# Optimization experiments

Measured on AMD Instinct MI355X. Metric: run time of the kernel, lower is better.

## Reference

```python
import jax, jax.numpy as jnp
import numpy as np

H, DK, DV = 4, 64, 64        # heads, key/value head dims (hidden=256)
M, TOPK = 4, 2               # num memories, router top-k
GN, EPS, COND_SCALE = 16.0, 1e-5, 1.0


def setup_inputs() -> dict:
    key = jax.random.key(0)
    ks = jax.random.split(key, 12)
    B, Q, K, D = 8, 64, 256, 256
    w = lambda k, shape, fan: jax.random.normal(k, shape, jnp.float32) / np.sqrt(fan).astype(np.float32)
    return {
        "query": jax.random.normal(ks[0], (B, Q, D), jnp.float32),
        "keyval": jax.random.normal(ks[1], (B, K, D), jnp.float32),
        "attention_mask_kv": jnp.ones((B, K), jnp.int32),
        "W_cond": w(ks[2], (D, D), D),
        "W_q": w(ks[3], (D, H * DK), D),
        "W_k": w(ks[4], (D, H * DK), D),
        "W_v": w(ks[5], (D, H * DV), D),
        "W_gk1": w(ks[6], (D, 16), D),
        "W_gk2": w(ks[7], (16, H * DK), 16),
        "b_gk2": jnp.zeros((H * DK,), jnp.float32),
        "W_router": w(ks[8], (D, M), D),
        "norm_w": jnp.ones((DV,), jnp.float32),
        "W_o": w(ks[9], (H * DV, D), H * DV),
    }


def _mem_last(q_last, k, v, gk, sel, wgt):
    """Last-token output of one gated linear-attention memory.
    S_t = diag(exp(gk_t)) S_{t-1} + k_t v_t^T ; o_T = q_T S_T.
    q_last: (N,H,DK); k,gk: (N,K,H,DK); v: (N,K,H,DV); sel,wgt: (N,K)."""
    k_e = k * sel[:, :, None, None]
    v_e = v * wgt[:, :, None, None]
    gk_e = gk * sel[:, :, None, None]          # unselected tokens: no decay, no update
    G = jnp.cumsum(gk_e, axis=1)               # (N,K,H,DK), log decays
    decay = jnp.exp(G[:, -1:, :, :] - G)       # remaining decay to last step, <= 1
    s = jnp.einsum('nhd,nthd->nth', q_last, k_e * decay)
    return jnp.einsum('nth,nthv->nhv', s, v_e)


def reference(query, keyval, attention_mask_kv, W_cond, W_q, W_k, W_v,
              W_gk1, W_gk2, b_gk2, W_router, norm_w, W_o):
    B, Q, D = query.shape
    K = keyval.shape[1]
    N = B * Q
    # broadcast KV expansion + cond injection
    cond = (query @ W_cond) * COND_SCALE                         # (B,Q,D)
    x = (keyval[:, None, :, :] + cond[:, :, None, :]).reshape(N, K, D)
    m = jnp.broadcast_to(attention_mask_kv[:, None, :].astype(x.dtype), (B, Q, K)).reshape(N, K)
    # projections
    q = (x @ W_q).reshape(N, K, H, DK)
    k = (x @ W_k).reshape(N, K, H, DK) * m[:, :, None, None]
    v = (x @ W_v).reshape(N, K, H, DV) * m[:, :, None, None]
    gk = (jax.nn.log_sigmoid(x @ W_gk1 @ W_gk2 + b_gk2) / GN).reshape(N, K, H, DK)
    gk = gk * m[:, :, None, None]
    # router: softmax -> top-k -> renormalize
    router_logits = (x @ W_router).reshape(N * K, M)
    probs = jax.nn.softmax(router_logits, axis=-1)
    topv, topi = jax.lax.top_k(probs, TOPK)
    topv = topv / jnp.sum(topv, axis=-1, keepdims=True)
    w_mem = jnp.sum(jax.nn.one_hot(topi, M, dtype=x.dtype) * topv[..., None], axis=-2)
    w_mem = w_mem.reshape(N, K, M)
    # shared memory (always on) + routed memories
    q_last = q[:, -1]
    ones = jnp.ones((N, K), x.dtype)
    o = _mem_last(q_last, k, v, gk, ones, ones)
    for e in range(M):
        we = w_mem[:, :, e]
        o = o + _mem_last(q_last, k, v, gk, (we > 0).astype(x.dtype), we)
    # per-head RMSNorm + output projection
    o = o * jax.lax.rsqrt(jnp.mean(o * o, axis=-1, keepdims=True) + EPS) * norm_w
    out = (o.reshape(N, H * DV) @ W_o).reshape(B, Q, D)
    return out, router_logits
```

## Files before the change

kernel.cpp:

```cpp
#include <hip/hip_runtime.h>
#include <math.h>

#define Hh   4
#define Bb   8
#define Qq   64
#define Kk   256
#define Dd   256
#define Nn   (Bb * Qq)
#define GNf  16.0f
#define EPSf 1e-5f

#define SKV  832
#define SCB  1088

__device__ __forceinline__ float wred(float x) {
#pragma unroll
    for (int off = 32; off > 0; off >>= 1)
        x += __shfl_xor(x, off, 64);
    return x;
}

__global__ __launch_bounds__(256) void prep(
    const float* __restrict__ Wg1, const float* __restrict__ Wg2,
    float* __restrict__ Wg)
{
    const int e = blockIdx.x * 256 + threadIdx.x;
    const int k = e >> 8, c = e & 255;
    float s = 0.f;
#pragma unroll
    for (int i = 0; i < 16; ++i)
        s = fmaf(Wg1[k * 16 + i], Wg2[i * 256 + c], s);
    Wg[e] = s;
}

__device__ __forceinline__ void gemm_tile(
    const float* __restrict__ A, int lda, int Mv,
    const float* __restrict__ B, int ldb, int bn,
    float* __restrict__ C, int ldc)
{
    __shared__ float As[16][68];
    __shared__ float Ws[16][136];
    const int tid = threadIdx.x;
    const int ty = tid >> 4, tx = tid & 15;
    const int am = tid >> 2, ak = (tid & 3) << 2;
    const int wk = tid >> 4, wc = (tid & 15) << 3;
    const int ams = (am < Mv) ? am : (Mv - 1);

    float acc[4][8] = {};

    const float* aptr = A + (size_t)ams * lda + ak;
    const float* bptr = B + (size_t)wk * ldb + bn + wc;
    float4 av  = *(const float4*)(aptr);
    float4 bv0 = *(const float4*)(bptr);
    float4 bv1 = *(const float4*)(bptr + 4);

    for (int k0 = 0; k0 < 256; k0 += 16) {
        __syncthreads();
        As[ak + 0][am] = av.x;
        As[ak + 1][am] = av.y;
        As[ak + 2][am] = av.z;
        As[ak + 3][am] = av.w;
        *(float4*)&Ws[wk][wc]     = bv0;
        *(float4*)&Ws[wk][wc + 4] = bv1;
        __syncthreads();
        if (k0 + 16 < 256) {
            av  = *(const float4*)(aptr + k0 + 16);
            bv0 = *(const float4*)(bptr + (size_t)(k0 + 16) * ldb);
            bv1 = *(const float4*)(bptr + (size_t)(k0 + 16) * ldb + 4);
        }
#pragma unroll
        for (int kk = 0; kk < 16; ++kk) {
            const float4 a4 = *(const float4*)&As[kk][ty << 2];
            const float4 w0 = *(const float4*)&Ws[kk][tx << 2];
            const float4 w1 = *(const float4*)&Ws[kk][64 + (tx << 2)];
            const float a_[4] = {a4.x, a4.y, a4.z, a4.w};
            const float w_[8] = {w0.x, w0.y, w0.z, w0.w, w1.x, w1.y, w1.z, w1.w};
#pragma unroll
            for (int i = 0; i < 4; ++i)
#pragma unroll
                for (int jj = 0; jj < 8; ++jj)
                    acc[i][jj] = fmaf(a_[i], w_[jj], acc[i][jj]);
        }
    }

#pragma unroll
    for (int i = 0; i < 4; ++i) {
        const int rr = (ty << 2) + i;
        if (rr < Mv) {
            *(float4*)(C + (size_t)rr * ldc + (tx << 2)) =
                make_float4(acc[i][0], acc[i][1], acc[i][2], acc[i][3]);
            *(float4*)(C + (size_t)rr * ldc + 64 + (tx << 2)) =
                make_float4(acc[i][4], acc[i][5], acc[i][6], acc[i][7]);
        }
    }
}

__device__ __forceinline__ void router_region(
    const float* __restrict__ A, const float* __restrict__ Wr,
    float* __restrict__ C, int ldc, int row0)
{
    __shared__ float WrT[4][260];
    const int tid = threadIdx.x;
    for (int idx = tid; idx < 1024; idx += 256) {
        const int k = idx >> 2, c = idx & 3;
        WrT[c][k] = Wr[idx];
    }
    __syncthreads();
    const int row = row0 + (tid >> 2), c = tid & 3;
    const float* a = A + (size_t)row * 256;
    float acc = 0.f;
#pragma unroll 8
    for (int k4 = 0; k4 < 64; ++k4) {
        const float4 avv = *(const float4*)(a + (k4 << 2));
        const float4 wvv = *(const float4*)&WrT[c][k4 << 2];
        acc = fmaf(avv.x, wvv.x, acc);
        acc = fmaf(avv.y, wvv.y, acc);
        acc = fmaf(avv.z, wvv.z, acc);
        acc = fmaf(avv.w, wvv.w, acc);
    }
    C[(size_t)row * ldc + c] = acc;
}

__global__ __launch_bounds__(256) void gemm_main(
    const float* __restrict__ keyval, const float* __restrict__ query,
    const float* __restrict__ W_k, const float* __restrict__ W_v,
    const float* __restrict__ Wg, const float* __restrict__ W_cond,
    const float* __restrict__ W_q, const float* __restrict__ W_router,
    float* __restrict__ KVb, float* __restrict__ cond,
    float* __restrict__ qlast)
{
    const int id = blockIdx.x;
    if (id < 242 - 32) {
        const float* A; int lda, Mv; const float* Bm; int bn; float* C; int ldc;
        if (id < 192) {
            const int rt = id / 6, ct = id % 6;
            const float* Bsel; int cbase;
            if (ct < 2)      { Bsel = W_k; cbase = 0; }
            else if (ct < 4) { Bsel = W_v; cbase = 256; }
            else             { Bsel = Wg;  cbase = 512; }
            A = keyval + (size_t)rt * 64 * 256; lda = 256; Mv = 64;
            Bm = Bsel; bn = (ct & 1) * 128;
            C = KVb + (size_t)rt * 64 * SKV + cbase + bn; ldc = SKV;
        } else if (id < 208) {
            const int t = id - 192, rt = t >> 1, ct = t & 1;
            A = query + (size_t)rt * 64 * 256; lda = 256; Mv = 64;
            Bm = W_cond; bn = ct * 128;
            C = cond + (size_t)rt * 64 * 256 + ct * 128; ldc = 256;
        } else {
            const int ct = id - 208;
            A = keyval + 255 * 256; lda = Kk * Dd; Mv = 8;
            Bm = W_q; bn = ct * 128;
            C = qlast + ct * 128; ldc = 256;
        }
        gemm_tile(A, lda, Mv, Bm, 256, bn, C, ldc);
    } else {
        router_region(keyval, W_router, KVb + 768, SKV, (id - 210) * 64);
    }
}

__global__ __launch_bounds__(256) void gemm_cb(
    const float* __restrict__ cond,
    const float* __restrict__ W_q, const float* __restrict__ W_k,
    const float* __restrict__ W_v, const float* __restrict__ Wg,
    const float* __restrict__ W_router, float* __restrict__ Cb)
{
    const int id = blockIdx.x;
    if (id < 64) {
        const int rg = id >> 4, t = id & 15, rt = t >> 1, ct = t & 1;
        const float* Bsel = (rg == 0) ? W_q : (rg == 1) ? W_k : (rg == 2) ? W_v : Wg;
        gemm_tile(cond + (size_t)rt * 64 * 256, 256, 64,
                  Bsel, 256, ct * 128,
                  Cb + (size_t)rt * 64 * SCB + rg * 256 + ct * 128, SCB);
    } else {
        router_region(cond, W_router, Cb + 1024, SCB, (id - 64) * 64);
    }
}

__global__ __launch_bounds__(256) void mom_fused(
    const float* __restrict__ KVb, const float* __restrict__ Cb,
    const float* __restrict__ qlast, const float* __restrict__ b_gk2,
    const int* __restrict__ mask, const float* __restrict__ W_o,
    const float* __restrict__ norm_w, float* __restrict__ out,
    float* __restrict__ logits)
{
    __shared__ float4 wm[Kk];
    __shared__ float4 sw[Kk];
    __shared__ float  smf[Kk];
    __shared__ float  Ptile[4][16][68];
    __shared__ float  sbuf[4][16];
    __shared__ float  onorm[Dd];

    const int bid = blockIdx.x;
    const int n = ((bid & 7) << 6) | (bid >> 3);
    const int b = n >> 6;
    const int j = threadIdx.x;
    const int lane = j & 63;
    const int wv = j >> 6;

    const float qc = Cb[(size_t)n * SCB + j];
    const float kc = Cb[(size_t)n * SCB + 256 + j];
    const float vc = Cb[(size_t)n * SCB + 512 + j];
    const float pc = Cb[(size_t)n * SCB + 768 + j] + b_gk2[j];
    const float4 rc = *(const float4*)(Cb + (size_t)n * SCB + 1024);

    const int* pm = mask + b * Kk;

    {
        const float4 kvr = *(const float4*)(KVb + (size_t)(b * Kk + j) * SKV + 768);
        float l[4] = {kvr.x + rc.x, kvr.y + rc.y, kvr.z + rc.z, kvr.w + rc.w};
        *(float4*)(logits + ((size_t)n * Kk + j) * 4) = make_float4(l[0], l[1], l[2], l[3]);

        int i1 = 0;
#pragma unroll
        for (int q = 1; q < 4; ++q) if (l[q] > l[i1]) i1 = q;
        int i2 = -1;
#pragma unroll
        for (int q = 0; q < 4; ++q) {
            if (q == i1) continue;
            if (i2 < 0 || l[q] > l[i2]) i2 = q;
        }
        const float mx = fmaxf(l[i1], l[i2]);
        const float e1 = __expf(l[i1] - mx);
        const float e2 = __expf(l[i2] - mx);
        const float inv = 1.f / (e1 + e2);
        float w[4] = {0.f, 0.f, 0.f, 0.f};
        w[i1] = e1 * inv;
        w[i2] = e2 * inv;
        wm[j] = make_float4(w[0], w[1], w[2], w[3]);
        const float mfj = (float)pm[j];
        smf[j] = mfj;
        sw[j] = make_float4(w[0] > 0.f ? mfj : 0.f, w[1] > 0.f ? mfj : 0.f,
                            w[2] > 0.f ? mfj : 0.f, w[3] > 0.f ? mfj : 0.f);
    }
    __syncthreads();

    const float ql  = qlast[b * Dd + j] + qc;
    const float qkc = ql * kc;
    const float* pkv = KVb + (size_t)b * Kk * SKV + j;

    float E0 = 1.f, E1 = 1.f, E2 = 1.f, E3 = 1.f, E4 = 1.f;
    float o = 0.f;
    const int tl = lane & 15, qq = lane >> 4;

    for (int t0 = Kk - 16; t0 >= 0; t0 -= 16) {
        float vreg[16];
#pragma unroll
        for (int i = 0; i < 16; ++i) {
            const int t = t0 + 15 - i;
            const float* r = pkv + (size_t)t * SKV;
            const float kraw = r[0];
            const float vraw = r[256];
            const float praw = r[512];
            const float pre = praw + pc;
            const float ee = __expf(-pre);
            const float dg = __expf(-0.0625f * __logf(1.0f + ee));
            const float4 w  = wm[t];
            const float4 s4 = sw[t];
            const float mf  = smf[t];
            const float zf = E0 + w.x * E1 + w.y * E2 + w.z * E3 + w.w * E4;
            const float qlk = fmaf(ql, kraw, qkc);
            Ptile[wv][i][lane] = qlk * zf * mf;
            vreg[i] = vraw + vc;
            const float d1 = dg - 1.0f;
            E0 *= fmaf(mf,   d1, 1.0f);
            E1 *= fmaf(s4.x, d1, 1.0f);
            E2 *= fmaf(s4.y, d1, 1.0f);
            E3 *= fmaf(s4.z, d1, 1.0f);
            E4 *= fmaf(s4.w, d1, 1.0f);
        }
        __builtin_amdgcn_wave_barrier();

        float s = 0.f;
#pragma unroll
        for (int rr = 0; rr < 4; ++rr) {
            const float4 p4 = *(const float4*)&Ptile[wv][tl][qq * 16 + rr * 4];
            s += (p4.x + p4.y) + (p4.z + p4.w);
        }
        s += __shfl_xor(s, 16, 64);
        s += __shfl_xor(s, 32, 64);
        sbuf[wv][tl] = s;
        __builtin_amdgcn_wave_barrier();
#pragma unroll
        for (int rr = 0; rr < 4; ++rr) {
            const float4 sv = *(const float4*)&sbuf[wv][rr * 4];
            o = fmaf(sv.x, vreg[rr * 4 + 0], o);
            o = fmaf(sv.y, vreg[rr * 4 + 1], o);
            o = fmaf(sv.z, vreg[rr * 4 + 2], o);
            o = fmaf(sv.w, vreg[rr * 4 + 3], o);
        }
    }

    const float ms = wred(o * o) * (1.0f / 64.0f);
    onorm[j] = o * rsqrtf(ms + EPSf) * norm_w[lane];
    __syncthreads();

    float acc = 0.f;
#pragma unroll 8
    for (int k = 0; k < Dd; ++k)
        acc = fmaf(onorm[k], W_o[(size_t)k * Dd + j], acc);
    out[(size_t)n * Dd + j] = acc;
}

extern "C" void kernel_launch(void* const* d_in, const int* in_sizes, int n_in,
                              void* d_out, int out_size, void* d_ws, size_t ws_size,
                              hipStream_t stream)
{
    const float* query    = (const float*)d_in[0];
    const float* keyval   = (const float*)d_in[1];
    const int*   mask     = (const int*)  d_in[2];
    const float* W_cond   = (const float*)d_in[3];
    const float* W_q      = (const float*)d_in[4];
    const float* W_k      = (const float*)d_in[5];
    const float* W_v      = (const float*)d_in[6];
    const float* W_gk1    = (const float*)d_in[7];
    const float* W_gk2    = (const float*)d_in[8];
    const float* b_gk2    = (const float*)d_in[9];
    const float* W_router = (const float*)d_in[10];
    const float* norm_w   = (const float*)d_in[11];
    const float* W_o      = (const float*)d_in[12];

    float* out    = (float*)d_out;
    float* logits = out + Nn * Dd;

    float* p = (float*)d_ws;
    float* Wg    = p; p += 256 * 256;
    float* KVb   = p; p += 2048 * SKV;
    float* cond  = p; p += Nn * 256;
    float* qlast = p; p += 8 * 256;
    float* Cb    = p; p += Nn * SCB;

    prep<<<256, dim3(256), 0, stream>>>(W_gk1, W_gk2, Wg);

    gemm_main<<<242, dim3(256), 0, stream>>>(
        keyval, query, W_k, W_v, Wg, W_cond, W_q, W_router, KVb, cond, qlast);

    gemm_cb<<<72, dim3(256), 0, stream>>>(cond, W_q, W_k, W_v, Wg, W_router, Cb);

    mom_fused<<<Nn, dim3(256), 0, stream>>>(
        KVb, Cb, qlast, b_gk2, mask, W_o, norm_w, out, logits);
}
```

Measured before the change: 206.0 us.

## Fuse all stages into one persistent kernel with software grid barriers

Merges the weight-prep, the keyval/cond projection GEMMs and the memory recurrence into a single 512-block kernel. Stages are separated by atomic-counter grid barriers, and shared memory is shared through a union. The projection GEMMs move to 128x128 tiles, and the gating selection masks are now computed inline instead of staged through shared arrays. This removes three launch boundaries and the tail gaps between them. In exchange it relies on all 512 blocks being co-resident (launch_bounds 256,2) to avoid deadlock, and leaves many blocks idle during the early phases.

```diff
diff --git a/kernel.cpp b/kernel.cpp
--- a/kernel.cpp
+++ b/kernel.cpp
@@ -10,8 +10,19 @@
 #define GNf  16.0f
 #define EPSf 1e-5f
 
-#define SKV  832
-#define SCB  1088
+#define SKV  776
+#define SCB  1032
+#define GRID 512
+
+struct MomS {
+    float4 wm[Kk];
+    float  Pt[4][16][68];
+    float  sbuf[4][16];
+    float  onorm[Dd];
+};
+struct GemmS { float As[16][136]; float Ws[16][136]; };
+struct RtrS  { float WrT[4][260]; };
+union  AllS  { MomS m; GemmS g; RtrS r; };
 
 __device__ __forceinline__ float wred(float x) {
 #pragma unroll
@@ -20,26 +31,24 @@
     return x;
 }
 
-__global__ __launch_bounds__(256) void prep(
-    const float* __restrict__ Wg1, const float* __restrict__ Wg2,
-    float* __restrict__ Wg)
-{
-    const int e = blockIdx.x * 256 + threadIdx.x;
-    const int k = e >> 8, c = e & 255;
-    float s = 0.f;
-#pragma unroll
-    for (int i = 0; i < 16; ++i)
-        s = fmaf(Wg1[k * 16 + i], Wg2[i * 256 + c], s);
-    Wg[e] = s;
-}
-
-__device__ __forceinline__ void gemm_tile(
-    const float* __restrict__ A, int lda, int Mv,
-    const float* __restrict__ B, int ldb, int bn,
-    float* __restrict__ C, int ldc)
-{
-    __shared__ float As[16][68];
-    __shared__ float Ws[16][136];
+__device__ __forceinline__ void gridbar(unsigned* cnt, unsigned nblk) {
+    __threadfence();
+    __syncthreads();
+    if (threadIdx.x == 0) {
+        __hip_atomic_fetch_add(cnt, 1u, __ATOMIC_ACQ_REL, __HIP_MEMORY_SCOPE_AGENT);
+        while (__hip_atomic_load(cnt, __ATOMIC_ACQUIRE, __HIP_MEMORY_SCOPE_AGENT)
+               < nblk)
+            __builtin_amdgcn_s_sleep(1);
+    }
+    __syncthreads();
+    __threadfence();
+}
+
+__device__ void gemm64(GemmS& g, const float* __restrict__ A, int lda, int Mv,
+                       const float* __restrict__ B, int bn,
+                       float* __restrict__ C, int ldc)
+{
+    float (*As)[68] = (float(*)[68])(&g.As[0][0]);
     const int tid = threadIdx.x;
     const int ty = tid >> 4, tx = tid & 15;
     const int am = tid >> 2, ak = (tid & 3) << 2;
@@ -47,32 +56,29 @@
     const int ams = (am < Mv) ? am : (Mv - 1);
 
     float acc[4][8] = {};
-
     const float* aptr = A + (size_t)ams * lda + ak;
-    const float* bptr = B + (size_t)wk * ldb + bn + wc;
-    float4 av  = *(const float4*)(aptr);
-    float4 bv0 = *(const float4*)(bptr);
-    float4 bv1 = *(const float4*)(bptr + 4);
+    const float* bptr = B + wk * 256 + bn + wc;
+    float4 av = *(const float4*)aptr;
+    float4 b0 = *(const float4*)bptr;
+    float4 b1 = *(const float4*)(bptr + 4);
 
     for (int k0 = 0; k0 < 256; k0 += 16) {
         __syncthreads();
-        As[ak + 0][am] = av.x;
-        As[ak + 1][am] = av.y;
-        As[ak + 2][am] = av.z;
-        As[ak + 3][am] = av.w;
-        *(float4*)&Ws[wk][wc]     = bv0;
-        *(float4*)&Ws[wk][wc + 4] = bv1;
+        As[ak + 0][am] = av.x; As[ak + 1][am] = av.y;
+        As[ak + 2][am] = av.z; As[ak + 3][am] = av.w;
+        *(float4*)&g.Ws[wk][wc]     = b0;
+        *(float4*)&g.Ws[wk][wc + 4] = b1;
         __syncthreads();
         if (k0 + 16 < 256) {
-            av  = *(const float4*)(aptr + k0 + 16);
-            bv0 = *(const float4*)(bptr + (size_t)(k0 + 16) * ldb);
-            bv1 = *(const float4*)(bptr + (size_t)(k0 + 16) * ldb + 4);
+            av = *(const float4*)(aptr + k0 + 16);
+            b0 = *(const float4*)(bptr + (k0 + 16) * 256);
+            b1 = *(const float4*)(bptr + (k0 + 16) * 256 + 4);
         }
 #pragma unroll
         for (int kk = 0; kk < 16; ++kk) {
             const float4 a4 = *(const float4*)&As[kk][ty << 2];
-            const float4 w0 = *(const float4*)&Ws[kk][tx << 2];
-            const float4 w1 = *(const float4*)&Ws[kk][64 + (tx << 2)];
+            const float4 w0 = *(const float4*)&g.Ws[kk][tx << 2];
+            const float4 w1 = *(const float4*)&g.Ws[kk][64 + (tx << 2)];
             const float a_[4] = {a4.x, a4.y, a4.z, a4.w};
             const float w_[8] = {w0.x, w0.y, w0.z, w0.w, w1.x, w1.y, w1.z, w1.w};
 #pragma unroll
@@ -95,16 +101,69 @@
     }
 }
 
-__device__ __forceinline__ void router_region(
-    const float* __restrict__ A, const float* __restrict__ Wr,
-    float* __restrict__ C, int ldc, int row0)
-{
-    __shared__ float WrT[4][260];
+__device__ void gemm128(GemmS& g, const float* __restrict__ A,
+                        const float* __restrict__ B, int bn,
+                        float* __restrict__ C, int ldc)
+{
     const int tid = threadIdx.x;
-    for (int idx = tid; idx < 1024; idx += 256) {
-        const int k = idx >> 2, c = idx & 3;
-        WrT[c][k] = Wr[idx];
-    }
+    const int ty = tid >> 4, tx = tid & 15;
+    const int am = tid >> 1, ak = (tid & 1) << 3;
+    const int wk = tid >> 4, wc = (tid & 15) << 3;
+
+    float acc[8][8] = {};
+    const float* aptr = A + (size_t)am * 256 + ak;
+    const float* bptr = B + wk * 256 + bn + wc;
+    float4 a0 = *(const float4*)aptr;
+    float4 a1 = *(const float4*)(aptr + 4);
+    float4 b0 = *(const float4*)bptr;
+    float4 b1 = *(const float4*)(bptr + 4);
+
+    for (int k0 = 0; k0 < 256; k0 += 16) {
+        __syncthreads();
+        g.As[ak + 0][am] = a0.x; g.As[ak + 1][am] = a0.y;
+        g.As[ak + 2][am] = a0.z; g.As[ak + 3][am] = a0.w;
+        g.As[ak + 4][am] = a1.x; g.As[ak + 5][am] = a1.y;
+        g.As[ak + 6][am] = a1.z; g.As[ak + 7][am] = a1.w;
+        *(float4*)&g.Ws[wk][wc]     = b0;
+        *(float4*)&g.Ws[wk][wc + 4] = b1;
+        __syncthreads();
+        if (k0 + 16 < 256) {
+            a0 = *(const float4*)(aptr + k0 + 16);
+            a1 = *(const float4*)(aptr + k0 + 20);
+            b0 = *(const float4*)(bptr + (k0 + 16) * 256);
+            b1 = *(const float4*)(bptr + (k0 + 16) * 256 + 4);
+        }
+#pragma unroll
+        for (int kk = 0; kk < 16; ++kk) {
+            const float4 x0 = *(const float4*)&g.As[kk][ty << 3];
+            const float4 x1 = *(const float4*)&g.As[kk][(ty << 3) + 4];
+            const float4 y0 = *(const float4*)&g.Ws[kk][tx << 3];
+            const float4 y1 = *(const float4*)&g.Ws[kk][(tx << 3) + 4];
+            const float xa[8] = {x0.x, x0.y, x0.z, x0.w, x1.x, x1.y, x1.z, x1.w};
+            const float yb[8] = {y0.x, y0.y, y0.z, y0.w, y1.x, y1.y, y1.z, y1.w};
+#pragma unroll
+            for (int i = 0; i < 8; ++i)
+#pragma unroll
+                for (int jj = 0; jj < 8; ++jj)
+                    acc[i][jj] = fmaf(xa[i], yb[jj], acc[i][jj]);
+        }
+    }
+
+#pragma unroll
+    for (int i = 0; i < 8; ++i) {
+        float* cr = C + (size_t)((ty << 3) + i) * ldc + (tx << 3);
+        *(float4*)cr       = make_float4(acc[i][0], acc[i][1], acc[i][2], acc[i][3]);
+        *(float4*)(cr + 4) = make_float4(acc[i][4], acc[i][5], acc[i][6], acc[i][7]);
+    }
+}
+
+__device__ void router_region(RtrS& rs, const float* __restrict__ A,
+                              const float* __restrict__ Wr,
+                              float* __restrict__ C, int ldc, int row0)
+{
+    const int tid = threadIdx.x;
+    for (int idx = tid; idx < 1024; idx += 256)
+        rs.WrT[idx & 3][idx >> 2] = Wr[idx];
     __syncthreads();
     const int row = row0 + (tid >> 2), c = tid & 3;
     const float* a = A + (size_t)row * 256;
@@ -112,7 +171,7 @@
 #pragma unroll 8
     for (int k4 = 0; k4 < 64; ++k4) {
         const float4 avv = *(const float4*)(a + (k4 << 2));
-        const float4 wvv = *(const float4*)&WrT[c][k4 << 2];
+        const float4 wvv = *(const float4*)&rs.WrT[c][k4 << 2];
         acc = fmaf(avv.x, wvv.x, acc);
         acc = fmaf(avv.y, wvv.y, acc);
         acc = fmaf(avv.z, wvv.z, acc);
@@ -121,77 +180,83 @@
     C[(size_t)row * ldc + c] = acc;
 }
 
-__global__ __launch_bounds__(256) void gemm_main(
-    const float* __restrict__ keyval, const float* __restrict__ query,
-    const float* __restrict__ W_k, const float* __restrict__ W_v,
-    const float* __restrict__ Wg, const float* __restrict__ W_cond,
-    const float* __restrict__ W_q, const float* __restrict__ W_router,
-    float* __restrict__ KVb, float* __restrict__ cond,
-    float* __restrict__ qlast)
-{
-    const int id = blockIdx.x;
-    if (id < 242 - 32) {
-        const float* A; int lda, Mv; const float* Bm; int bn; float* C; int ldc;
-        if (id < 192) {
-            const int rt = id / 6, ct = id % 6;
-            const float* Bsel; int cbase;
-            if (ct < 2)      { Bsel = W_k; cbase = 0; }
-            else if (ct < 4) { Bsel = W_v; cbase = 256; }
-            else             { Bsel = Wg;  cbase = 512; }
-            A = keyval + (size_t)rt * 64 * 256; lda = 256; Mv = 64;
-            Bm = Bsel; bn = (ct & 1) * 128;
-            C = KVb + (size_t)rt * 64 * SKV + cbase + bn; ldc = SKV;
-        } else if (id < 208) {
-            const int t = id - 192, rt = t >> 1, ct = t & 1;
-            A = query + (size_t)rt * 64 * 256; lda = 256; Mv = 64;
-            Bm = W_cond; bn = ct * 128;
-            C = cond + (size_t)rt * 64 * 256 + ct * 128; ldc = 256;
-        } else {
-            const int ct = id - 208;
-            A = keyval + 255 * 256; lda = Kk * Dd; Mv = 8;
-            Bm = W_q; bn = ct * 128;
-            C = qlast + ct * 128; ldc = 256;
-        }
-        gemm_tile(A, lda, Mv, Bm, 256, bn, C, ldc);
-    } else {
-        router_region(keyval, W_router, KVb + 768, SKV, (id - 210) * 64);
-    }
-}
-
-__global__ __launch_bounds__(256) void gemm_cb(
-    const float* __restrict__ cond,
+__device__ void wg_region(const float* __restrict__ Wg1,
+                          const float* __restrict__ Wg2,
+                          float* __restrict__ Wg, int k0)
+{
+    const int c = threadIdx.x;
+    float w2[16];
+#pragma unroll
+    for (int i = 0; i < 16; ++i) w2[i] = Wg2[i * 256 + c];
+#pragma unroll
+    for (int r = 0; r < 16; ++r) {
+        const int k = k0 + r;
+        float s = 0.f;
+#pragma unroll
+        for (int i = 0; i < 16; ++i) s = fmaf(Wg1[k * 16 + i], w2[i], s);
+        Wg[k * 256 + c] = s;
+    }
+}
+
+__global__ __launch_bounds__(256, 2) void fused_all(
+    const float* __restrict__ query, const float* __restrict__ keyval,
+    const int* __restrict__ mask, const float* __restrict__ W_cond,
     const float* __restrict__ W_q, const float* __restrict__ W_k,
-    const float* __restrict__ W_v, const float* __restrict__ Wg,
-    const float* __restrict__ W_router, float* __restrict__ Cb)
-{
-    const int id = blockIdx.x;
-    if (id < 64) {
-        const int rg = id >> 4, t = id & 15, rt = t >> 1, ct = t & 1;
-        const float* Bsel = (rg == 0) ? W_q : (rg == 1) ? W_k : (rg == 2) ? W_v : Wg;
-        gemm_tile(cond + (size_t)rt * 64 * 256, 256, 64,
-                  Bsel, 256, ct * 128,
-                  Cb + (size_t)rt * 64 * SCB + rg * 256 + ct * 128, SCB);
-    } else {
-        router_region(cond, W_router, Cb + 1024, SCB, (id - 64) * 64);
-    }
-}
-
-__global__ __launch_bounds__(256) void mom_fused(
-    const float* __restrict__ KVb, const float* __restrict__ Cb,
-    const float* __restrict__ qlast, const float* __restrict__ b_gk2,
-    const int* __restrict__ mask, const float* __restrict__ W_o,
-    const float* __restrict__ norm_w, float* __restrict__ out,
-    float* __restrict__ logits)
-{
-    __shared__ float4 wm[Kk];
-    __shared__ float4 sw[Kk];
-    __shared__ float  smf[Kk];
-    __shared__ float  Ptile[4][16][68];
-    __shared__ float  sbuf[4][16];
-    __shared__ float  onorm[Dd];
-
+    const float* __restrict__ W_v, const float* __restrict__ W_gk1,
+    const float* __restrict__ W_gk2, const float* __restrict__ b_gk2,
+    const float* __restrict__ W_router, const float* __restrict__ norm_w,
+    const float* __restrict__ W_o,
+    float* __restrict__ Wg, float* __restrict__ KVb, float* __restrict__ cond,
+    float* __restrict__ qlast, float* __restrict__ Cb,
+    float* __restrict__ out, float* __restrict__ logits,
+    unsigned* __restrict__ bar)
+{
+    __shared__ AllS S;
     const int bid = blockIdx.x;
-    const int n = ((bid & 7) << 6) | (bid >> 3);
+
+    if (bid % 7 == 0) {
+        const int jj = bid / 7;
+        if (jj < 16) {
+            wg_region(W_gk1, W_gk2, Wg, jj * 16);
+        } else if (jj < 32) {
+            const int t = jj - 16;
+            gemm64(S.g, query + (size_t)(t >> 1) * 64 * 256, 256, 64,
+                   W_cond, (t & 1) * 128,
+                   cond + (size_t)(t >> 1) * 64 * 256 + (t & 1) * 128, 256);
+        } else if (jj < 34) {
+            gemm64(S.g, keyval + 255 * 256, Kk * Dd, 8, W_q, (jj - 32) * 128,
+                   qlast + (jj - 32) * 128, 256);
+        } else if (jj < 66) {
+            router_region(S.r, keyval, W_router, KVb + 768, SKV, (jj - 34) * 64);
+        }
+    }
+    gridbar(&bar[0], GRID);
+
+    if (bid < 256) {
+        if ((bid & 1) == 0) {
+            const int jj = bid >> 1;
+            if (jj < 96) {
+                const int rt = jj / 6, ct = jj % 6;
+                const float* Bsel = (ct < 2) ? W_k : (ct < 4) ? W_v : Wg;
+                gemm128(S.g, keyval + (size_t)rt * 128 * 256, Bsel, (ct & 1) * 128,
+                        KVb + (size_t)rt * 128 * SKV + (ct >> 1) * 256
+                            + (ct & 1) * 128, SKV);
+            } else {
+                const int t = jj - 96, rt = t >> 3, ct = t & 7;
+                const float* Bsel = (ct < 2) ? W_q : (ct < 4) ? W_k
+                                  : (ct < 6) ? W_v : Wg;
+                gemm128(S.g, cond + (size_t)rt * 128 * 256, Bsel, (ct & 1) * 128,
+                        Cb + (size_t)rt * 128 * SCB + (ct >> 1) * 256
+                           + (ct & 1) * 128, SCB);
+            }
+        } else if (bid < 16) {
+            router_region(S.r, cond, W_router, Cb + 1024, SCB,
+                          ((bid - 1) >> 1) * 64);
+        }
+    }
+    gridbar(&bar[1], GRID);
+
+    const int n = bid;
     const int b = n >> 6;
     const int j = threadIdx.x;
     const int lane = j & 63;
@@ -208,7 +273,8 @@
     {
         const float4 kvr = *(const float4*)(KVb + (size_t)(b * Kk + j) * SKV + 768);
         float l[4] = {kvr.x + rc.x, kvr.y + rc.y, kvr.z + rc.z, kvr.w + rc.w};
-        *(float4*)(logits + ((size_t)n * Kk + j) * 4) = make_float4(l[0], l[1], l[2], l[3]);
+        *(float4*)(logits + ((size_t)n * Kk + j) * 4) =
+            make_float4(l[0], l[1], l[2], l[3]);
 
         int i1 = 0;
 #pragma unroll
@@ -226,21 +292,17 @@
         float w[4] = {0.f, 0.f, 0.f, 0.f};
         w[i1] = e1 * inv;
         w[i2] = e2 * inv;
-        wm[j] = make_float4(w[0], w[1], w[2], w[3]);
-        const float mfj = (float)pm[j];
-        smf[j] = mfj;
-        sw[j] = make_float4(w[0] > 0.f ? mfj : 0.f, w[1] > 0.f ? mfj : 0.f,
-                            w[2] > 0.f ? mfj : 0.f, w[3] > 0.f ? mfj : 0.f);
-    }
-    __syncthreads();
-
-    const float ql  = qlast[b * Dd + j] + qc;
+        S.m.wm[j] = make_float4(w[0], w[1], w[2], w[3]);
+    }
+    __syncthreads();
+
+    const float ql  = qlast[b * 256 + j] + qc;
     const float qkc = ql * kc;
     const float* pkv = KVb + (size_t)b * Kk * SKV + j;
 
     float E0 = 1.f, E1 = 1.f, E2 = 1.f, E3 = 1.f, E4 = 1.f;
     float o = 0.f;
-    const int tl = lane & 15, qq = lane >> 4;
+    const int tl = lane & 15, qg = lane >> 4;
 
     for (int t0 = Kk - 16; t0 >= 0; t0 -= 16) {
         float vreg[16];
@@ -251,54 +313,53 @@
             const float kraw = r[0];
             const float vraw = r[256];
             const float praw = r[512];
+            const float mf  = (float)pm[t];
             const float pre = praw + pc;
-            const float ee = __expf(-pre);
-            const float dg = __expf(-0.0625f * __logf(1.0f + ee));
-            const float4 w  = wm[t];
-            const float4 s4 = sw[t];
-            const float mf  = smf[t];
+            const float ee  = __expf(-pre);
+            float dg = __expf(-0.0625f * __logf(1.f + ee));
+            dg = (mf != 0.f) ? dg : 1.f;
+            const float4 w = S.m.wm[t];
             const float zf = E0 + w.x * E1 + w.y * E2 + w.z * E3 + w.w * E4;
             const float qlk = fmaf(ql, kraw, qkc);
-            Ptile[wv][i][lane] = qlk * zf * mf;
+            S.m.Pt[wv][i][lane] = qlk * zf * mf;
             vreg[i] = vraw + vc;
-            const float d1 = dg - 1.0f;
-            E0 *= fmaf(mf,   d1, 1.0f);
-            E1 *= fmaf(s4.x, d1, 1.0f);
-            E2 *= fmaf(s4.y, d1, 1.0f);
-            E3 *= fmaf(s4.z, d1, 1.0f);
-            E4 *= fmaf(s4.w, d1, 1.0f);
+            E0 *= dg;
+            E1 *= (w.x > 0.f) ? dg : 1.f;
+            E2 *= (w.y > 0.f) ? dg : 1.f;
+            E3 *= (w.z > 0.f) ? dg : 1.f;
+            E4 *= (w.w > 0.f) ? dg : 1.f;
         }
         __builtin_amdgcn_wave_barrier();
 
         float s = 0.f;
 #pragma unroll
-        for (int rr = 0; rr < 4; ++rr) {
-            const float4 p4 = *(const float4*)&Ptile[wv][tl][qq * 16 + rr * 4];
+        for (int rr4 = 0; rr4 < 4; ++rr4) {
+            const float4 p4 = *(const float4*)&S.m.Pt[wv][tl][qg * 16 + rr4 * 4];
             s += (p4.x + p4.y) + (p4.z + p4.w);
         }
         s += __shfl_xor(s, 16, 64);
         s += __shfl_xor(s, 32, 64);
-        sbuf[wv][tl] = s;
+        S.m.sbuf[wv][tl] = s;
         __builtin_amdgcn_wave_barrier();
 #pragma unroll
-        for (int rr = 0; rr < 4; ++rr) {
-            const float4 sv = *(const float4*)&sbuf[wv][rr * 4];
-            o = fmaf(sv.x, vreg[rr * 4 + 0], o);
-            o = fmaf(sv.y, vreg[rr * 4 + 1], o);
-            o = fmaf(sv.z, vreg[rr * 4 + 2], o);
-            o = fmaf(sv.w, vreg[rr * 4 + 3], o);
+        for (int rr4 = 0; rr4 < 4; ++rr4) {
+            const float4 sv = *(const float4*)&S.m.sbuf[wv][rr4 * 4];
+            o = fmaf(sv.x, vreg[rr4 * 4 + 0], o);
+            o = fmaf(sv.y, vreg[rr4 * 4 + 1], o);
+            o = fmaf(sv.z, vreg[rr4 * 4 + 2], o);
+            o = fmaf(sv.w, vreg[rr4 * 4 + 3], o);
         }
     }
 
     const float ms = wred(o * o) * (1.0f / 64.0f);
-    onorm[j] = o * rsqrtf(ms + EPSf) * norm_w[lane];
+    S.m.onorm[j] = o * rsqrtf(ms + EPSf) * norm_w[lane];
     __syncthreads();
 
     float acc = 0.f;
 #pragma unroll 8
-    for (int k = 0; k < Dd; ++k)
-        acc = fmaf(onorm[k], W_o[(size_t)k * Dd + j], acc);
-    out[(size_t)n * Dd + j] = acc;
+    for (int k = 0; k < 256; ++k)
+        acc = fmaf(S.m.onorm[k], W_o[(size_t)k * 256 + j], acc);
+    out[(size_t)n * 256 + j] = acc;
 }
 
 extern "C" void kernel_launch(void* const* d_in, const int* in_sizes, int n_in,
@@ -328,14 +389,11 @@
     float* cond  = p; p += Nn * 256;
     float* qlast = p; p += 8 * 256;
     float* Cb    = p; p += Nn * SCB;
-
-    prep<<<256, dim3(256), 0, stream>>>(W_gk1, W_gk2, Wg);
-
-    gemm_main<<<242, dim3(256), 0, stream>>>(
-        keyval, query, W_k, W_v, Wg, W_cond, W_q, W_router, KVb, cond, qlast);
-
-    gemm_cb<<<72, dim3(256), 0, stream>>>(cond, W_q, W_k, W_v, Wg, W_router, Cb);
-
-    mom_fused<<<Nn, dim3(256), 0, stream>>>(
-        KVb, Cb, qlast, b_gk2, mask, W_o, norm_w, out, logits);
-}
+    unsigned* bar = (unsigned*)p;
+
+    hipMemsetAsync(bar, 0, 256, stream);
+    fused_all<<<dim3(GRID), dim3(256), 0, stream>>>(
+        query, keyval, mask, W_cond, W_q, W_k, W_v, W_gk1, W_gk2, b_gk2,
+        W_router, norm_w, W_o,
+        Wg, KVb, cond, qlast, Cb, out, logits, bar);
+}
```

Result: slower. 450.0 us (+118.5%).
